# Kernel optimization log

Measured on AMD Instinct MI355X. Metric: run time of the kernel, lower is better.

## Reference

```python
import jax, jax.numpy as jnp
import numpy as np

N = 512        # neuron_number
F = 256        # input_size
K = 6          # unfolding_steps
B, T = 128, 256


def setup_inputs() -> dict:
    key = jax.random.key(0)
    k1, k2, k3, k4, k5, k6, k7 = jax.random.split(key, 7)
    i = jax.random.normal(k1, (B, T, F), dtype=jnp.float32)
    delta_t = jax.random.uniform(k2, (B, T), dtype=jnp.float32)  # positive dt
    # LiquidCell parameters
    W_rec = jax.random.normal(k3, (N, N), dtype=jnp.float32) / np.sqrt(N)
    W_in = jax.random.normal(k4, (N, F), dtype=jnp.float32) / np.sqrt(F)
    b = jax.random.normal(k5, (N,), dtype=jnp.float32) * 0.01
    A = jax.random.normal(k6, (N,), dtype=jnp.float32)
    tau = jax.random.uniform(k7, (N,), dtype=jnp.float32, minval=0.5, maxval=1.5)
    return {"i": i, "delta_t": delta_t, "W_rec": W_rec, "W_in": W_in,
            "b": b, "A": A, "tau": tau}


def _cell(x, i_t, dt, W_rec, W_in, b, A, tau):
    # Fused semi-implicit LTC solver, unfolded K times. x:[B,N] i_t:[B,F] dt:[B]
    dt_k = (dt / K)[:, None]                      # [B,1]
    inp_part = i_t @ W_in.T + b                   # [B,N], constant across unfolding
    for _ in range(K):
        f = jnp.tanh(x @ W_rec.T + inp_part)      # [B,N]
        x = (x + dt_k * f * A) / (1.0 + dt_k * (1.0 / tau + f))
    return x


def reference(i, delta_t, W_rec, W_in, b, A, tau):
    batch = i.shape[0]
    x0 = jnp.tanh(jnp.zeros((batch, N), dtype=i.dtype))  # _get_first_x

    def step(x, ts):
        i_t, dt = ts
        x_new = _cell(x, i_t, dt, W_rec, W_in, b, A, tau)
        return x_new, x_new

    xs = (jnp.swapaxes(i, 0, 1), delta_t.T)       # time-major: [T,B,F], [T,B]
    _, ys = jax.lax.scan(step, x0, xs)            # ys: [T,B,N]
    return jnp.swapaxes(ys, 0, 1)                 # [B,T,N] (stacked outputs)
```

## Files before the change

kernel.cpp:

```cpp
#include <hip/hip_runtime.h>
#include <math.h>

typedef unsigned long long ull;


#define NN 512
#define FF 256
#define KK 6
#define BB 128
#define TT 256
#define BT 2
#define NTL 128

#define XROW 512
#define IPITCH 260
#define WIPITCH 260
#define PPITCH 17

#define DOT4(a, v) ((a).x * (v).x + (a).y * (v).y + (a).z * (v).z + (a).w * (v).w)

__global__ __launch_bounds__(512, 2) void liquid_kernel(
    const float* __restrict__ I,
    const float* __restrict__ DT,
    const float* __restrict__ Wrec,
    const float* __restrict__ Win,
    const float* __restrict__ bv, const float* __restrict__ Av,
    const float* __restrict__ tauv,
    ull* __restrict__ mbx,
    float* __restrict__ out)
{
  __shared__ __align__(16) float lds[39178];
  float* xsh = lds;
  float* iro = lds + BT * XROW;
  float* wi  = iro + BT * IPITCH;
  float* par = wi + NTL * WIPITCH;
  float* dts = par + 256 * PPITCH;

  const int blk = blockIdx.x;
  const int bt  = blk >> 2;
  const int nt  = blk & 3;
  const int tid = threadIdx.x;
  const int kc  = tid & 15;
  const int nq  = tid >> 4;
  const int n0g = nt * NTL;

  float4 wv[4][8];
  #pragma unroll
  for (int r = 0; r < 4; ++r) {
    const float* wr = Wrec + (size_t)(n0g + nq * 4 + r) * NN + kc * 32;
    #pragma unroll
    for (int j = 0; j < 8; ++j) wv[r][j] = *(const float4*)(wr + 4 * j);
  }
  for (int idx = tid; idx < NTL * FF; idx += 512) {
    const int n = idx >> 8, f = idx & 255;
    const int g = f >> 2, gs = g ^ ((g >> 3) & 7);
    wi[n * WIPITCH + gs * 4 + (f & 3)] = Win[(size_t)(n0g + n) * FF + f];
  }
  float rA = 0.f, rIT = 0.f, rB = 0.f;
  int swn = 0;
  if (tid < 256) {
    const int rn = tid & 127;
    const int n = n0g + rn;
    rA = Av[n]; rIT = 1.0f / tauv[n]; rB = bv[n];
    const int gg = n >> 2;
    swn = ((gg ^ ((gg >> 3) & 7)) << 2) | (n & 3);
  }
  for (int idx = tid; idx < BT * XROW; idx += 512) xsh[idx] = 0.f;

  const int sx  = kc & 7;
  const int gb  = (kc * 4) ^ ((kc >> 1) & 7);
  const float4* xq0 = (const float4*)xsh + kc * 8;
  const float4* xq1 = xq0 + 128;
  const float4* iq0 = (const float4*)iro;
  const float4* iq1 = iq0 + 65;
  const float4* wq  = (const float4*)wi + (nq * 4) * 65;
  const int stb = tid >> 8;
  const int stn = 2 * (tid & 255);
  const int stg = stn >> 2;
  float* stw = xsh + stb * XROW + ((stg ^ ((stg >> 3) & 7)) << 2) + (stn & 3);
  __syncthreads();

  int jj = 0;
  #pragma unroll 1
  for (int t = 0; t < TT; ++t) {
    if (tid < 2 * 64) {
      const int b = tid >> 6, f4 = tid & 63;
      const int gsi = f4 ^ ((f4 >> 3) & 7);
      ((float4*)iro)[b * 65 + gsi] =
          *(const float4*)&I[((size_t)(bt * BT + b) * TT + t) * FF + f4 * 4];
    }
    if (tid < BT) dts[tid] = DT[(size_t)(bt * BT + tid) * TT + t] * (1.0f / KK);
    __syncthreads();

    {
      float ai0[4] = {0.f, 0.f, 0.f, 0.f}, ai1[4] = {0.f, 0.f, 0.f, 0.f};
      #pragma unroll
      for (int j2 = 0; j2 < 4; ++j2) {
        const int gg = gb ^ j2;
        float4 w0 = wq[0 * 65 + gg];
        float4 w1 = wq[1 * 65 + gg];
        float4 w2 = wq[2 * 65 + gg];
        float4 w3 = wq[3 * 65 + gg];
        float4 xa = iq0[gg];
        float4 xb = iq1[gg];
        ai0[0] += DOT4(w0, xa); ai0[1] += DOT4(w1, xa);
        ai0[2] += DOT4(w2, xa); ai0[3] += DOT4(w3, xa);
        ai1[0] += DOT4(w0, xb); ai1[1] += DOT4(w1, xb);
        ai1[2] += DOT4(w2, xb); ai1[3] += DOT4(w3, xb);
      }
      #pragma unroll
      for (int r = 0; r < 4; ++r) {
        par[(0 * NTL + nq * 4 + r) * PPITCH + kc] = ai0[r];
        par[(1 * NTL + nq * 4 + r) * PPITCH + kc] = ai1[r];
      }
    }
    __syncthreads();
    float rInp = 0.f;
    if (tid < 256) {
      float s = rB;
      #pragma unroll
      for (int c = 0; c < 16; ++c) s += par[tid * PPITCH + c];
      rInp = s;
    }
    __syncthreads();

    #pragma unroll 1
    for (int kk = 0; kk < KK; ++kk) {
      ++jj;

      if (jj > 1) {
        const ull* src = mbx + (((size_t)bt * 2 + ((jj - 1) & 1)) << 10);
        const ull* p = src + 2 * tid;
        const unsigned want = (unsigned)(jj - 1);
        ull v0 = __hip_atomic_load(p,     __ATOMIC_RELAXED, __HIP_MEMORY_SCOPE_AGENT);
        ull v1 = __hip_atomic_load(p + 1, __ATOMIC_RELAXED, __HIP_MEMORY_SCOPE_AGENT);
        while ((unsigned)(v0 >> 32) != want || (unsigned)(v1 >> 32) != want) {
          __builtin_amdgcn_s_sleep(1);
          if ((unsigned)(v0 >> 32) != want)
            v0 = __hip_atomic_load(p,     __ATOMIC_RELAXED, __HIP_MEMORY_SCOPE_AGENT);
          if ((unsigned)(v1 >> 32) != want)
            v1 = __hip_atomic_load(p + 1, __ATOMIC_RELAXED, __HIP_MEMORY_SCOPE_AGENT);
        }
        stw[0] = __uint_as_float((unsigned)v0);
        stw[1] = __uint_as_float((unsigned)v1);
      }
      __syncthreads();

      {
        float acc0[4] = {0.f, 0.f, 0.f, 0.f}, acc1[4] = {0.f, 0.f, 0.f, 0.f};
        #pragma unroll
        for (int j = 0; j < 8; ++j) {
          float4 xv = xq0[j ^ sx];
          acc0[0] += DOT4(wv[0][j], xv); acc0[1] += DOT4(wv[1][j], xv);
          acc0[2] += DOT4(wv[2][j], xv); acc0[3] += DOT4(wv[3][j], xv);
        }
        #pragma unroll
        for (int j = 0; j < 8; ++j) {
          float4 xv = xq1[j ^ sx];
          acc1[0] += DOT4(wv[0][j], xv); acc1[1] += DOT4(wv[1][j], xv);
          acc1[2] += DOT4(wv[2][j], xv); acc1[3] += DOT4(wv[3][j], xv);
        }
        #pragma unroll
        for (int r = 0; r < 4; ++r) {
          par[(0 * NTL + nq * 4 + r) * PPITCH + kc] = acc0[r];
          par[(1 * NTL + nq * 4 + r) * PPITCH + kc] = acc1[r];
        }
      }
      __syncthreads();

      if (tid < 256) {
        float arg = rInp;
        #pragma unroll
        for (int c = 0; c < 16; ++c) arg += par[tid * PPITCH + c];
        const int rb = tid >> 7, rn = tid & 127;
        float f   = tanhf(arg);
        float dtk = dts[rb];
        float xo  = xsh[rb * XROW + swn];
        float xn  = fmaf(dtk * f, rA, xo) / fmaf(dtk, rIT + f, 1.0f);
        ull w = ((ull)(unsigned)jj << 32) | (ull)__float_as_uint(xn);
        __hip_atomic_store(mbx + (((size_t)bt * 2 + (jj & 1)) << 10) + rb * 512 + n0g + rn,
                           w, __ATOMIC_RELAXED, __HIP_MEMORY_SCOPE_AGENT);
        if (kk == KK - 1)
          out[((size_t)(bt * BT + rb) * TT + t) * NN + n0g + rn] = xn;
      }
      __syncthreads();
    }
  }
}

extern "C" void kernel_launch(void* const* d_in, const int* in_sizes, int n_in,
                              void* d_out, int out_size, void* d_ws, size_t ws_size,
                              hipStream_t stream) {
  const float* I    = (const float*)d_in[0];
  const float* DT   = (const float*)d_in[1];
  const float* Wrec = (const float*)d_in[2];
  const float* Win  = (const float*)d_in[3];
  const float* bv   = (const float*)d_in[4];
  const float* Av   = (const float*)d_in[5];
  const float* tauv = (const float*)d_in[6];
  float* out = (float*)d_out;
  ull* mbx = (ull*)d_ws;

  liquid_kernel<<<256, 512, 0, stream>>>(I, DT, Wrec, Win, bv, Av, tauv, mbx, out);
}
```

Measured before the change: 3.474 ms.

## Replace LDS partial-sum reduction with wave shuffles and double-buffer state locally

Partial dot products over the 16 k-chunks are now reduced with xor-shuffles inside each wavefront instead of being written to a shared partial array and summed by 256 threads. That removes the partial array and one barrier per unfolding step plus two per timestep. The recurrent state is double-buffered in LDS, and each block writes its own neurons locally, so it only polls the mailbox for the neurons owned by other blocks. A bounded spin guard is added to the poll loop. The costs are more shuffle instructions, a serial select chain, and half the lanes idle in the epilogue.

```diff
diff --git a/kernel.cpp b/kernel.cpp
--- a/kernel.cpp
+++ b/kernel.cpp
@@ -7,15 +7,13 @@
 #define NN 512
 #define FF 256
 #define KK 6
-#define BB 128
 #define TT 256
 #define BT 2
 #define NTL 128
 
-#define XROW 512
 #define IPITCH 260
 #define WIPITCH 260
-#define PPITCH 17
+#define XBUF (BT * NN)
 
 #define DOT4(a, v) ((a).x * (v).x + (a).y * (v).y + (a).z * (v).z + (a).w * (v).w)
 
@@ -29,12 +27,11 @@
     ull* __restrict__ mbx,
     float* __restrict__ out)
 {
-  __shared__ __align__(16) float lds[39178];
+  __shared__ __align__(16) float lds[2 * XBUF + BT * IPITCH + NTL * WIPITCH + 8];
   float* xsh = lds;
-  float* iro = lds + BT * XROW;
+  float* iro = lds + 2 * XBUF;
   float* wi  = iro + BT * IPITCH;
-  float* par = wi + NTL * WIPITCH;
-  float* dts = par + 256 * PPITCH;
+  float* dts = wi + NTL * WIPITCH;
 
   const int blk = blockIdx.x;
   const int bt  = blk >> 2;
@@ -56,34 +53,33 @@
     const int g = f >> 2, gs = g ^ ((g >> 3) & 7);
     wi[n * WIPITCH + gs * 4 + (f & 3)] = Win[(size_t)(n0g + n) * FF + f];
   }
+  const int bm = kc >> 2;
+  const int nm = n0g + nq * 4 + (kc & 3);
   float rA = 0.f, rIT = 0.f, rB = 0.f;
   int swn = 0;
-  if (tid < 256) {
-    const int rn = tid & 127;
-    const int n = n0g + rn;
-    rA = Av[n]; rIT = 1.0f / tauv[n]; rB = bv[n];
-    const int gg = n >> 2;
-    swn = ((gg ^ ((gg >> 3) & 7)) << 2) | (n & 3);
-  }
-  for (int idx = tid; idx < BT * XROW; idx += 512) xsh[idx] = 0.f;
+  if (kc < 8) {
+    rA = Av[nm]; rIT = 1.0f / tauv[nm]; rB = bv[nm];
+    const int gg = nm >> 2;
+    swn = ((gg ^ ((gg >> 3) & 7)) << 2) | (nm & 3);
+  }
+  for (int idx = tid; idx < 2 * XBUF; idx += 512) xsh[idx] = 0.f;
 
   const int sx  = kc & 7;
   const int gb  = (kc * 4) ^ ((kc >> 1) & 7);
-  const float4* xq0 = (const float4*)xsh + kc * 8;
-  const float4* xq1 = xq0 + 128;
   const float4* iq0 = (const float4*)iro;
   const float4* iq1 = iq0 + 65;
   const float4* wq  = (const float4*)wi + (nq * 4) * 65;
   const int stb = tid >> 8;
   const int stn = 2 * (tid & 255);
+  const bool rem = (stn < n0g) || (stn >= n0g + NTL);
   const int stg = stn >> 2;
-  float* stw = xsh + stb * XROW + ((stg ^ ((stg >> 3) & 7)) << 2) + (stn & 3);
+  const int sts = ((stg ^ ((stg >> 3) & 7)) << 2) | (stn & 3);
   __syncthreads();
 
   int jj = 0;
   #pragma unroll 1
   for (int t = 0; t < TT; ++t) {
-    if (tid < 2 * 64) {
+    if (tid < 128) {
       const int b = tid >> 6, f4 = tid & 63;
       const int gsi = f4 ^ ((f4 >> 3) & 7);
       ((float4*)iro)[b * 65 + gsi] =
@@ -92,8 +88,9 @@
     if (tid < BT) dts[tid] = DT[(size_t)(bt * BT + tid) * TT + t] * (1.0f / KK);
     __syncthreads();
 
+    float rInp = 0.f, dtk = 0.f;
     {
-      float ai0[4] = {0.f, 0.f, 0.f, 0.f}, ai1[4] = {0.f, 0.f, 0.f, 0.f};
+      float ai[8] = {0.f, 0.f, 0.f, 0.f, 0.f, 0.f, 0.f, 0.f};
       #pragma unroll
       for (int j2 = 0; j2 < 4; ++j2) {
         const int gg = gb ^ j2;
@@ -103,87 +100,94 @@
         float4 w3 = wq[3 * 65 + gg];
         float4 xa = iq0[gg];
         float4 xb = iq1[gg];
-        ai0[0] += DOT4(w0, xa); ai0[1] += DOT4(w1, xa);
-        ai0[2] += DOT4(w2, xa); ai0[3] += DOT4(w3, xa);
-        ai1[0] += DOT4(w0, xb); ai1[1] += DOT4(w1, xb);
-        ai1[2] += DOT4(w2, xb); ai1[3] += DOT4(w3, xb);
+        ai[0] += DOT4(w0, xa); ai[1] += DOT4(w1, xa);
+        ai[2] += DOT4(w2, xa); ai[3] += DOT4(w3, xa);
+        ai[4] += DOT4(w0, xb); ai[5] += DOT4(w1, xb);
+        ai[6] += DOT4(w2, xb); ai[7] += DOT4(w3, xb);
       }
       #pragma unroll
-      for (int r = 0; r < 4; ++r) {
-        par[(0 * NTL + nq * 4 + r) * PPITCH + kc] = ai0[r];
-        par[(1 * NTL + nq * 4 + r) * PPITCH + kc] = ai1[r];
+      for (int s = 1; s <= 8; s <<= 1) {
+        #pragma unroll
+        for (int i = 0; i < 8; ++i) ai[i] += __shfl_xor(ai[i], s);
+      }
+      if (kc < 8) {
+        float a0 = (kc & 1) ? ai[1] : ai[0];
+        float a1 = (kc & 1) ? ai[3] : ai[2];
+        float a2 = (kc & 1) ? ai[5] : ai[4];
+        float a3 = (kc & 1) ? ai[7] : ai[6];
+        float b0 = (kc & 2) ? a1 : a0;
+        float b1 = (kc & 2) ? a3 : a2;
+        rInp = rB + ((kc & 4) ? b1 : b0);
+        dtk = dts[bm];
       }
     }
-    __syncthreads();
-    float rInp = 0.f;
-    if (tid < 256) {
-      float s = rB;
-      #pragma unroll
-      for (int c = 0; c < 16; ++c) s += par[tid * PPITCH + c];
-      rInp = s;
-    }
-    __syncthreads();
 
     #pragma unroll 1
     for (int kk = 0; kk < KK; ++kk) {
       ++jj;
-
-      if (jj > 1) {
-        const ull* src = mbx + (((size_t)bt * 2 + ((jj - 1) & 1)) << 10);
-        const ull* p = src + 2 * tid;
+      const int rp = (jj - 1) & 1;
+      const int wp = jj & 1;
+
+      if (jj > 1 && rem) {
+        const ull* p = mbx + (((size_t)bt * 2 + rp) << 10) + 2 * tid;
         const unsigned want = (unsigned)(jj - 1);
         ull v0 = __hip_atomic_load(p,     __ATOMIC_RELAXED, __HIP_MEMORY_SCOPE_AGENT);
         ull v1 = __hip_atomic_load(p + 1, __ATOMIC_RELAXED, __HIP_MEMORY_SCOPE_AGENT);
-        while ((unsigned)(v0 >> 32) != want || (unsigned)(v1 >> 32) != want) {
+        int guard = 1 << 16;
+        while (((unsigned)(v0 >> 32) != want || (unsigned)(v1 >> 32) != want)
+               && --guard) {
           __builtin_amdgcn_s_sleep(1);
           if ((unsigned)(v0 >> 32) != want)
             v0 = __hip_atomic_load(p,     __ATOMIC_RELAXED, __HIP_MEMORY_SCOPE_AGENT);
           if ((unsigned)(v1 >> 32) != want)
             v1 = __hip_atomic_load(p + 1, __ATOMIC_RELAXED, __HIP_MEMORY_SCOPE_AGENT);
         }
-        stw[0] = __uint_as_float((unsigned)v0);
-        stw[1] = __uint_as_float((unsigned)v1);
+        float* d = xsh + rp * XBUF + stb * NN;
+        d[sts]     = __uint_as_float((unsigned)v0);
+        d[sts + 1] = __uint_as_float((unsigned)v1);
       }
       __syncthreads();
 
+      float acc[8] = {0.f, 0.f, 0.f, 0.f, 0.f, 0.f, 0.f, 0.f};
       {
-        float acc0[4] = {0.f, 0.f, 0.f, 0.f}, acc1[4] = {0.f, 0.f, 0.f, 0.f};
+        const float4* x0 = (const float4*)xsh + rp * (XBUF / 4) + kc * 8;
+        const float4* x1 = x0 + 128;
         #pragma unroll
         for (int j = 0; j < 8; ++j) {
-          float4 xv = xq0[j ^ sx];
-          acc0[0] += DOT4(wv[0][j], xv); acc0[1] += DOT4(wv[1][j], xv);
-          acc0[2] += DOT4(wv[2][j], xv); acc0[3] += DOT4(wv[3][j], xv);
+          float4 xv = x0[j ^ sx];
+          acc[0] += DOT4(wv[0][j], xv); acc[1] += DOT4(wv[1][j], xv);
+          acc[2] += DOT4(wv[2][j], xv); acc[3] += DOT4(wv[3][j], xv);
         }
         #pragma unroll
         for (int j = 0; j < 8; ++j) {
-          float4 xv = xq1[j ^ sx];
-          acc1[0] += DOT4(wv[0][j], xv); acc1[1] += DOT4(wv[1][j], xv);
-          acc1[2] += DOT4(wv[2][j], xv); acc1[3] += DOT4(wv[3][j], xv);
+          float4 xv = x1[j ^ sx];
+          acc[4] += DOT4(wv[0][j], xv); acc[5] += DOT4(wv[1][j], xv);
+          acc[6] += DOT4(wv[2][j], xv); acc[7] += DOT4(wv[3][j], xv);
         }
-        #pragma unroll
-        for (int r = 0; r < 4; ++r) {
-          par[(0 * NTL + nq * 4 + r) * PPITCH + kc] = acc0[r];
-          par[(1 * NTL + nq * 4 + r) * PPITCH + kc] = acc1[r];
-        }
-      }
-      __syncthreads();
-
-      if (tid < 256) {
-        float arg = rInp;
-        #pragma unroll
-        for (int c = 0; c < 16; ++c) arg += par[tid * PPITCH + c];
-        const int rb = tid >> 7, rn = tid & 127;
+      }
+      #pragma unroll
+      for (int s = 1; s <= 8; s <<= 1) {
+        #pragma unroll
+        for (int i = 0; i < 8; ++i) acc[i] += __shfl_xor(acc[i], s);
+      }
+      if (kc < 8) {
+        float a0 = (kc & 1) ? acc[1] : acc[0];
+        float a1 = (kc & 1) ? acc[3] : acc[2];
+        float a2 = (kc & 1) ? acc[5] : acc[4];
+        float a3 = (kc & 1) ? acc[7] : acc[6];
+        float b0 = (kc & 2) ? a1 : a0;
+        float b1 = (kc & 2) ? a3 : a2;
+        float arg = rInp + ((kc & 4) ? b1 : b0);
         float f   = tanhf(arg);
-        float dtk = dts[rb];
-        float xo  = xsh[rb * XROW + swn];
+        float xo  = xsh[rp * XBUF + bm * NN + swn];
         float xn  = fmaf(dtk * f, rA, xo) / fmaf(dtk, rIT + f, 1.0f);
+        xsh[wp * XBUF + bm * NN + swn] = xn;
         ull w = ((ull)(unsigned)jj << 32) | (ull)__float_as_uint(xn);
-        __hip_atomic_store(mbx + (((size_t)bt * 2 + (jj & 1)) << 10) + rb * 512 + n0g + rn,
+        __hip_atomic_store(mbx + (((size_t)bt * 2 + wp) << 10) + bm * NN + nm,
                            w, __ATOMIC_RELAXED, __HIP_MEMORY_SCOPE_AGENT);
         if (kk == KK - 1)
-          out[((size_t)(bt * BT + rb) * TT + t) * NN + n0g + rn] = xn;
-      }
-      __syncthreads();
+          out[((size_t)(bt * BT + bm) * TT + t) * NN + nm] = xn;
+      }
     }
   }
 }
```

Measured after the change: 4.423 ms. 27.3% more time.

## Split neuron tiles eight ways and ping-pong two batch groups to hide exchange latency

Applied to the files above, without the earlier changes.

Each block now owns 64 neurons across 4 batch rows, handled as two interleaved batch pairs (A and B). While pair A's matvec and update run, the block prefetches pair B's remote state from the mailbox, and the reverse, so cross-block exchange latency overlaps with compute. Only slices owned by other blocks are fetched, since local results are written straight to LDS, and the spin-wait gets an iteration guard. This costs more synchronisation phases and a wider all-to-all among 8 blocks, and the guard can let stale data through if it expires.

```diff
diff --git a/kernel.cpp b/kernel.cpp
--- a/kernel.cpp
+++ b/kernel.cpp
@@ -7,17 +7,12 @@
 #define NN 512
 #define FF 256
 #define KK 6
-#define BB 128
 #define TT 256
-#define BT 2
-#define NTL 128
-
-#define XROW 512
-#define IPITCH 260
-#define WIPITCH 260
-#define PPITCH 17
+#define NTL 64
 
 #define DOT4(a, v) ((a).x * (v).x + (a).y * (v).y + (a).z * (v).z + (a).w * (v).w)
+#define MLOAD(q) __hip_atomic_load((q), __ATOMIC_RELAXED, __HIP_MEMORY_SCOPE_AGENT)
+#define MSTORE(q, x) __hip_atomic_store((q), (x), __ATOMIC_RELAXED, __HIP_MEMORY_SCOPE_AGENT)
 
 __global__ __launch_bounds__(512, 2) void liquid_kernel(
     const float* __restrict__ I,
@@ -29,161 +24,206 @@
     ull* __restrict__ mbx,
     float* __restrict__ out)
 {
-  __shared__ __align__(16) float lds[39178];
-  float* xsh = lds;
-  float* iro = lds + BT * XROW;
-  float* wi  = iro + BT * IPITCH;
-  float* par = wi + NTL * WIPITCH;
-  float* dts = par + 256 * PPITCH;
+  __shared__ __align__(16) float lds[24088];
+  float* xshA = lds;
+  float* xshB = lds + 1024;
+  float* iro  = lds + 2048;
+  float* wi   = iro + 4 * 260;
+  float* par  = wi + 64 * 260;
+  float* dts  = par + 256 * 17;
 
   const int blk = blockIdx.x;
-  const int bt  = blk >> 2;
-  const int nt  = blk & 3;
+  const int p   = blk >> 3;
+  const int nt  = blk & 7;
   const int tid = threadIdx.x;
   const int kc  = tid & 15;
   const int nq  = tid >> 4;
   const int n0g = nt * NTL;
-
-  float4 wv[4][8];
+  const int btA = 2 * p, btB = 2 * p + 1;
+
+  float4 wv[2][8];
   #pragma unroll
-  for (int r = 0; r < 4; ++r) {
-    const float* wr = Wrec + (size_t)(n0g + nq * 4 + r) * NN + kc * 32;
+  for (int r = 0; r < 2; ++r) {
+    const float* wr = Wrec + (size_t)(n0g + nq * 2 + r) * NN + kc * 32;
     #pragma unroll
     for (int j = 0; j < 8; ++j) wv[r][j] = *(const float4*)(wr + 4 * j);
   }
   for (int idx = tid; idx < NTL * FF; idx += 512) {
     const int n = idx >> 8, f = idx & 255;
     const int g = f >> 2, gs = g ^ ((g >> 3) & 7);
-    wi[n * WIPITCH + gs * 4 + (f & 3)] = Win[(size_t)(n0g + n) * FF + f];
+    wi[n * 260 + gs * 4 + (f & 3)] = Win[(size_t)(n0g + n) * FF + f];
   }
   float rA = 0.f, rIT = 0.f, rB = 0.f;
   int swn = 0;
   if (tid < 256) {
-    const int rn = tid & 127;
-    const int n = n0g + rn;
+    const int n = n0g + (tid & 63);
     rA = Av[n]; rIT = 1.0f / tauv[n]; rB = bv[n];
     const int gg = n >> 2;
     swn = ((gg ^ ((gg >> 3) & 7)) << 2) | (n & 3);
   }
-  for (int idx = tid; idx < BT * XROW; idx += 512) xsh[idx] = 0.f;
-
-  const int sx  = kc & 7;
-  const int gb  = (kc * 4) ^ ((kc >> 1) & 7);
-  const float4* xq0 = (const float4*)xsh + kc * 8;
-  const float4* xq1 = xq0 + 128;
-  const float4* iq0 = (const float4*)iro;
-  const float4* iq1 = iq0 + 65;
-  const float4* wq  = (const float4*)wi + (nq * 4) * 65;
-  const int stb = tid >> 8;
-  const int stn = 2 * (tid & 255);
-  const int stg = stn >> 2;
-  float* stw = xsh + stb * XROW + ((stg ^ ((stg >> 3) & 7)) << 2) + (stn & 3);
+  for (int idx = tid; idx < 2048; idx += 512) lds[idx] = 0.f;
+
+  const int sx = kc & 7;
+  const int gb = (kc * 4) ^ ((kc >> 1) & 7);
+  const float4* aq0 = (const float4*)xshA + kc * 8;
+  const float4* aq1 = aq0 + 128;
+  const float4* bq0 = (const float4*)xshB + kc * 8;
+  const float4* bq1 = bq0 + 128;
+  const float4* iq  = (const float4*)iro;
+  const float4* wq  = (const float4*)wi + (nq * 2) * 65;
+  const int sb = tid >> 8;
+  const int sn = 2 * (tid & 255);
+  const bool rem = (sn < n0g) || (sn >= n0g + NTL);
+  const int stg = sn >> 2;
+  const int sts = ((stg ^ ((stg >> 3) & 7)) << 2) | (sn & 3);
+  float* stwA = xshA + sb * 512 + sts;
+  float* stwB = xshB + sb * 512 + sts;
+  const int ment = sb * 512 + sn;
   __syncthreads();
 
-  int jj = 0;
+  int v = 0;
+  ull pA0 = 0, pA1 = 0, pB0 = 0, pB1 = 0;
   #pragma unroll 1
   for (int t = 0; t < TT; ++t) {
-    if (tid < 2 * 64) {
-      const int b = tid >> 6, f4 = tid & 63;
+    if (tid < 256) {
+      const int row = tid >> 6, f4 = tid & 63;
       const int gsi = f4 ^ ((f4 >> 3) & 7);
-      ((float4*)iro)[b * 65 + gsi] =
-          *(const float4*)&I[((size_t)(bt * BT + b) * TT + t) * FF + f4 * 4];
-    }
-    if (tid < BT) dts[tid] = DT[(size_t)(bt * BT + tid) * TT + t] * (1.0f / KK);
+      ((float4*)iro)[row * 65 + gsi] =
+          *(const float4*)&I[((size_t)(4 * p + row) * TT + t) * FF + f4 * 4];
+    }
+    if (tid < 4) dts[tid] = DT[(size_t)(4 * p + tid) * TT + t] * (1.0f / KK);
     __syncthreads();
 
     {
-      float ai0[4] = {0.f, 0.f, 0.f, 0.f}, ai1[4] = {0.f, 0.f, 0.f, 0.f};
+      float a00=0.f,a01=0.f,a10=0.f,a11=0.f,a20=0.f,a21=0.f,a30=0.f,a31=0.f;
       #pragma unroll
       for (int j2 = 0; j2 < 4; ++j2) {
         const int gg = gb ^ j2;
-        float4 w0 = wq[0 * 65 + gg];
-        float4 w1 = wq[1 * 65 + gg];
-        float4 w2 = wq[2 * 65 + gg];
-        float4 w3 = wq[3 * 65 + gg];
-        float4 xa = iq0[gg];
-        float4 xb = iq1[gg];
-        ai0[0] += DOT4(w0, xa); ai0[1] += DOT4(w1, xa);
-        ai0[2] += DOT4(w2, xa); ai0[3] += DOT4(w3, xa);
-        ai1[0] += DOT4(w0, xb); ai1[1] += DOT4(w1, xb);
-        ai1[2] += DOT4(w2, xb); ai1[3] += DOT4(w3, xb);
-      }
-      #pragma unroll
-      for (int r = 0; r < 4; ++r) {
-        par[(0 * NTL + nq * 4 + r) * PPITCH + kc] = ai0[r];
-        par[(1 * NTL + nq * 4 + r) * PPITCH + kc] = ai1[r];
-      }
+        float4 w0 = wq[gg], w1 = wq[65 + gg];
+        float4 x0 = iq[gg], x1 = iq[65 + gg], x2 = iq[130 + gg], x3 = iq[195 + gg];
+        a00 += DOT4(w0, x0); a01 += DOT4(w1, x0);
+        a10 += DOT4(w0, x1); a11 += DOT4(w1, x1);
+        a20 += DOT4(w0, x2); a21 += DOT4(w1, x2);
+        a30 += DOT4(w0, x3); a31 += DOT4(w1, x3);
+      }
+      const int pb = (nq * 2) * 17 + kc;
+      par[pb]            = a00; par[pb + 17]        = a01;
+      par[64 * 17 + pb]  = a10; par[64 * 17 + pb + 17]  = a11;
+      par[128 * 17 + pb] = a20; par[128 * 17 + pb + 17] = a21;
+      par[192 * 17 + pb] = a30; par[192 * 17 + pb + 17] = a31;
     }
     __syncthreads();
-    float rInp = 0.f;
+    float rInp = 0.f, dtk = 0.f;
     if (tid < 256) {
       float s = rB;
       #pragma unroll
-      for (int c = 0; c < 16; ++c) s += par[tid * PPITCH + c];
+      for (int c = 0; c < 16; ++c) s += par[tid * 17 + c];
       rInp = s;
-    }
-    __syncthreads();
+      dtk = dts[tid >> 6];
+    }
 
     #pragma unroll 1
     for (int kk = 0; kk < KK; ++kk) {
-      ++jj;
-
-      if (jj > 1) {
-        const ull* src = mbx + (((size_t)bt * 2 + ((jj - 1) & 1)) << 10);
-        const ull* p = src + 2 * tid;
-        const unsigned want = (unsigned)(jj - 1);
-        ull v0 = __hip_atomic_load(p,     __ATOMIC_RELAXED, __HIP_MEMORY_SCOPE_AGENT);
-        ull v1 = __hip_atomic_load(p + 1, __ATOMIC_RELAXED, __HIP_MEMORY_SCOPE_AGENT);
-        while ((unsigned)(v0 >> 32) != want || (unsigned)(v1 >> 32) != want) {
-          __builtin_amdgcn_s_sleep(1);
-          if ((unsigned)(v0 >> 32) != want)
-            v0 = __hip_atomic_load(p,     __ATOMIC_RELAXED, __HIP_MEMORY_SCOPE_AGENT);
-          if ((unsigned)(v1 >> 32) != want)
-            v1 = __hip_atomic_load(p + 1, __ATOMIC_RELAXED, __HIP_MEMORY_SCOPE_AGENT);
-        }
-        stw[0] = __uint_as_float((unsigned)v0);
-        stw[1] = __uint_as_float((unsigned)v1);
-      }
-      __syncthreads();
-
+      ++v;
+
+      if (v > 1 && rem) {
+        const unsigned want = (unsigned)(v - 1);
+        if ((unsigned)(pA0 >> 32) != want || (unsigned)(pA1 >> 32) != want) {
+          const ull* q = mbx + (((size_t)btA * 2 + ((v - 1) & 1)) << 10) + ment;
+          int guard = 1 << 14;
+          while (((unsigned)(pA0 >> 32) != want ||
+                  (unsigned)(pA1 >> 32) != want) && --guard) {
+            __builtin_amdgcn_s_sleep(1);
+            if ((unsigned)(pA0 >> 32) != want) pA0 = MLOAD(q);
+            if ((unsigned)(pA1 >> 32) != want) pA1 = MLOAD(q + 1);
+          }
+        }
+        stwA[0] = __uint_as_float((unsigned)pA0);
+        stwA[1] = __uint_as_float((unsigned)pA1);
+      }
+      __syncthreads();
+
+      if (v > 1 && rem) {
+        const ull* q = mbx + (((size_t)btB * 2 + ((v - 1) & 1)) << 10) + ment;
+        pB0 = MLOAD(q); pB1 = MLOAD(q + 1);
+      }
       {
-        float acc0[4] = {0.f, 0.f, 0.f, 0.f}, acc1[4] = {0.f, 0.f, 0.f, 0.f};
+        float c00=0.f,c01=0.f,c10=0.f,c11=0.f;
         #pragma unroll
         for (int j = 0; j < 8; ++j) {
-          float4 xv = xq0[j ^ sx];
-          acc0[0] += DOT4(wv[0][j], xv); acc0[1] += DOT4(wv[1][j], xv);
-          acc0[2] += DOT4(wv[2][j], xv); acc0[3] += DOT4(wv[3][j], xv);
-        }
+          float4 x0 = aq0[j ^ sx], x1 = aq1[j ^ sx];
+          c00 += DOT4(wv[0][j], x0); c01 += DOT4(wv[1][j], x0);
+          c10 += DOT4(wv[0][j], x1); c11 += DOT4(wv[1][j], x1);
+        }
+        const int pb = (nq * 2) * 17 + kc;
+        par[pb]           = c00; par[pb + 17]           = c01;
+        par[64 * 17 + pb] = c10; par[64 * 17 + pb + 17] = c11;
+      }
+      __syncthreads();
+
+      if (tid < 128) {
+        float arg = rInp;
+        #pragma unroll
+        for (int c = 0; c < 16; ++c) arg += par[tid * 17 + c];
+        const int b = tid >> 6, n = n0g + (tid & 63);
+        float f  = tanhf(arg);
+        float xo = xshA[b * 512 + swn];
+        float xn = fmaf(dtk * f, rA, xo) / fmaf(dtk, rIT + f, 1.0f);
+        xshA[b * 512 + swn] = xn;
+        MSTORE(mbx + (((size_t)btA * 2 + (v & 1)) << 10) + b * 512 + n,
+               ((ull)(unsigned)v << 32) | (ull)__float_as_uint(xn));
+        if (kk == KK - 1)
+          out[((size_t)(4 * p + b) * TT + t) * NN + n] = xn;
+      }
+      if (v > 1 && rem) {
+        const unsigned want = (unsigned)(v - 1);
+        if ((unsigned)(pB0 >> 32) != want || (unsigned)(pB1 >> 32) != want) {
+          const ull* q = mbx + (((size_t)btB * 2 + ((v - 1) & 1)) << 10) + ment;
+          int guard = 1 << 14;
+          while (((unsigned)(pB0 >> 32) != want ||
+                  (unsigned)(pB1 >> 32) != want) && --guard) {
+            __builtin_amdgcn_s_sleep(1);
+            if ((unsigned)(pB0 >> 32) != want) pB0 = MLOAD(q);
+            if ((unsigned)(pB1 >> 32) != want) pB1 = MLOAD(q + 1);
+          }
+        }
+        stwB[0] = __uint_as_float((unsigned)pB0);
+        stwB[1] = __uint_as_float((unsigned)pB1);
+      }
+      __syncthreads();
+
+      if (rem) {
+        const ull* q = mbx + (((size_t)btA * 2 + (v & 1)) << 10) + ment;
+        pA0 = MLOAD(q); pA1 = MLOAD(q + 1);
+      }
+      {
+        float c00=0.f,c01=0.f,c10=0.f,c11=0.f;
         #pragma unroll
         for (int j = 0; j < 8; ++j) {
-          float4 xv = xq1[j ^ sx];
-          acc1[0] += DOT4(wv[0][j], xv); acc1[1] += DOT4(wv[1][j], xv);
-          acc1[2] += DOT4(wv[2][j], xv); acc1[3] += DOT4(wv[3][j], xv);
-        }
-        #pragma unroll
-        for (int r = 0; r < 4; ++r) {
-          par[(0 * NTL + nq * 4 + r) * PPITCH + kc] = acc0[r];
-          par[(1 * NTL + nq * 4 + r) * PPITCH + kc] = acc1[r];
-        }
-      }
-      __syncthreads();
-
-      if (tid < 256) {
+          float4 x0 = bq0[j ^ sx], x1 = bq1[j ^ sx];
+          c00 += DOT4(wv[0][j], x0); c01 += DOT4(wv[1][j], x0);
+          c10 += DOT4(wv[0][j], x1); c11 += DOT4(wv[1][j], x1);
+        }
+        const int pb = (128 + nq * 2) * 17 + kc;
+        par[pb]           = c00; par[pb + 17]           = c01;
+        par[64 * 17 + pb] = c10; par[64 * 17 + pb + 17] = c11;
+      }
+      __syncthreads();
+
+      if (tid >= 128 && tid < 256) {
         float arg = rInp;
         #pragma unroll
-        for (int c = 0; c < 16; ++c) arg += par[tid * PPITCH + c];
-        const int rb = tid >> 7, rn = tid & 127;
-        float f   = tanhf(arg);
-        float dtk = dts[rb];
-        float xo  = xsh[rb * XROW + swn];
-        float xn  = fmaf(dtk * f, rA, xo) / fmaf(dtk, rIT + f, 1.0f);
-        ull w = ((ull)(unsigned)jj << 32) | (ull)__float_as_uint(xn);
-        __hip_atomic_store(mbx + (((size_t)bt * 2 + (jj & 1)) << 10) + rb * 512 + n0g + rn,
-                           w, __ATOMIC_RELAXED, __HIP_MEMORY_SCOPE_AGENT);
+        for (int c = 0; c < 16; ++c) arg += par[tid * 17 + c];
+        const int b = (tid >> 6) & 1, n = n0g + (tid & 63);
+        float f  = tanhf(arg);
+        float xo = xshB[b * 512 + swn];
+        float xn = fmaf(dtk * f, rA, xo) / fmaf(dtk, rIT + f, 1.0f);
+        xshB[b * 512 + swn] = xn;
+        MSTORE(mbx + (((size_t)btB * 2 + (v & 1)) << 10) + b * 512 + n,
+               ((ull)(unsigned)v << 32) | (ull)__float_as_uint(xn));
         if (kk == KK - 1)
-          out[((size_t)(bt * BT + rb) * TT + t) * NN + n0g + rn] = xn;
-      }
-      __syncthreads();
+          out[((size_t)(4 * p + 2 + b) * TT + t) * NN + n] = xn;
+      }
     }
   }
 }
```

After: 4.937 ms. +42.1%, slower.
